# Kernel optimization log

Measured on AMD Instinct MI355X. Metric: run time of the kernel, lower is better.

Reference implementation:

```python
import jax, jax.numpy as jnp
import numpy as np

B, S_BERT, L_WORD, D = 64, 512, 256, 768
REDUC, HID, TAGS, POL = 400, 100, 5, 4


def _make_positions():
    # Each word spans 1-2 consecutive subwords; 256 words * max 2 <= 512 subwords.
    rng = np.random.default_rng(0)
    lens = rng.integers(1, 3, size=(B, L_WORD))          # [B, L] in {1,2}
    starts = np.cumsum(lens, axis=1) - lens              # exclusive prefix sum
    ends = starts + lens - 1                             # inclusive end, <= 511
    return jnp.asarray(np.stack([starts, ends], axis=-1), dtype=jnp.int32)


def setup_inputs() -> dict:
    key = jax.random.key(0)
    ks = jax.random.split(key, 8)
    s = 0.02
    return {
        "bert_vectors": jax.random.normal(ks[0], (B, S_BERT, D), jnp.float32),
        "positions": _make_positions(),
        "W_reduc": jax.random.normal(ks[1], (D, REDUC), jnp.float32) * s,
        "b_reduc": jnp.zeros((REDUC,), jnp.float32),
        "W_ap": jax.random.normal(ks[2], (REDUC, HID), jnp.float32) * s,
        "b_ap": jnp.zeros((HID,), jnp.float32),
        "W_op": jax.random.normal(ks[3], (REDUC, HID), jnp.float32) * s,
        "b_op": jnp.zeros((HID,), jnp.float32),
        "W_ap_tag": jax.random.normal(ks[4], (HID, TAGS), jnp.float32) * s,
        "b_ap_tag": jnp.zeros((TAGS,), jnp.float32),
        "W_op_tag": jax.random.normal(ks[5], (HID, TAGS), jnp.float32) * s,
        "b_op_tag": jnp.zeros((TAGS,), jnp.float32),
        # Biaffine: bias=(True, False) -> in1 gets a ones column: [HID+1, POL*HID]
        "W_bi": jax.random.normal(ks[6], (HID + 1, POL * HID), jnp.float32) * s,
    }


def _segment_mean(vectors, positions):
    # vectors: [B, S, D]; positions: [B, L, 2] inclusive (start, end) spans.
    cs = jnp.cumsum(vectors, axis=1)
    cs = jnp.concatenate([jnp.zeros_like(cs[:, :1]), cs], axis=1)   # [B, S+1, D]
    starts = positions[..., 0]
    ends = positions[..., 1]
    hi = jnp.take_along_axis(cs, (ends + 1)[..., None], axis=1)     # [B, L, D]
    lo = jnp.take_along_axis(cs, starts[..., None], axis=1)
    lens = (ends - starts + 1).astype(vectors.dtype)[..., None]
    return (hi - lo) / lens                                          # [B, L, D]


def reference(bert_vectors, positions, W_reduc, b_reduc, W_ap, b_ap, W_op, b_op,
              W_ap_tag, b_ap_tag, W_op_tag, b_op_tag, W_bi):
    pooled = _segment_mean(bert_vectors, positions)                  # [B, L, D]
    h = jax.nn.relu(pooled @ W_reduc + b_reduc)                      # [B, L, 400]
    ap = jax.nn.relu(h @ W_ap + b_ap)                                # [B, L, 100]
    op = jax.nn.relu(h @ W_op + b_op)                                # [B, L, 100]
    ap_out = ap @ W_ap_tag + b_ap_tag                                # [B, L, T]
    op_out = op @ W_op_tag + b_op_tag                                # [B, L, T]
    # Biaffine with bias=(True, False)
    ones = jnp.ones_like(ap[..., :1])
    a1 = jnp.concatenate([ap, ones], axis=-1)                        # [B, L, 101]
    affine = (a1 @ W_bi).reshape(ap.shape[0], ap.shape[1], POL, HID) # [B, L1, P, H]
    triplet = jnp.einsum('biph,bjh->bjip', affine, op)               # [B, L2, L1, P]
    return ap_out, op_out, triplet
```

## Files before the change

kernel.cpp:

```cpp
#include <hip/hip_runtime.h>
#include <hip/hip_bf16.h>

#define B_    64
#define S_    512
#define L_    256
#define D_    768
#define RED_  400
#define REDP_ 512
#define KEFF_ 416
#define HID_  100
#define HIDP_ 128
#define TAGS_ 5
#define POL_  4
#define NBI_  512
#define NAO_  256
#define BL_   (B_ * L_)

typedef __attribute__((ext_vector_type(8))) short short8;
typedef __attribute__((ext_vector_type(4))) float f32x4;
typedef __attribute__((ext_vector_type(4))) unsigned short u16x4;

#define GLOAD_LDS16(gp, lp) __builtin_amdgcn_global_load_lds( \
    (const __attribute__((address_space(1))) void*)(gp),      \
    (__attribute__((address_space(3))) void*)(lp), 16, 0, 0)

__device__ inline float bf2f(unsigned short u) {
    union { unsigned int i; float f; } c; c.i = ((unsigned)u) << 16; return c.f;
}
__device__ inline unsigned short f2bf(float f) {
    __hip_bfloat16 h = __float2bfloat16(f);
    unsigned short u;
    __builtin_memcpy(&u, &h, 2);
    return u;
}

#define SZ0 393216
#define SZ1 131072
#define SZ2 65536
#define SZ3 512
#define SZ4 256
#define PREP_TOT (SZ0 + SZ1 + SZ2 + SZ3 + SZ4)
#define PREP_BLOCKS ((PREP_TOT + 255) / 256)

__global__ __launch_bounds__(256) void prep_kernel(
    const float* __restrict__ W_reduc, const float* __restrict__ b_reduc,
    const float* __restrict__ W_ap, const float* __restrict__ b_ap,
    const float* __restrict__ W_op, const float* __restrict__ b_op,
    const float* __restrict__ W_bi,
    unsigned short* __restrict__ WtR, unsigned short* __restrict__ WtAO,
    unsigned short* __restrict__ WtBi,
    float* __restrict__ bR, float* __restrict__ bAO, float* __restrict__ bBi)
{
    int idx = blockIdx.x * 256 + threadIdx.x;
    if (idx < SZ0) {
        int n = idx / D_, k = idx - n * D_;
        float v = (n < RED_) ? W_reduc[(size_t)k * RED_ + n] : 0.f;
        WtR[idx] = f2bf(v);
    } else if (idx < SZ0 + SZ1) {
        int i = idx - SZ0;
        int n = i >> 9, k = i & 511;
        float v = 0.f;
        if (k < RED_) {
            if (n < HID_)                      v = W_ap[(size_t)k * HID_ + n];
            else if (n >= 128 && n < 128+HID_) v = W_op[(size_t)k * HID_ + (n-128)];
        }
        WtAO[i] = f2bf(v);
    } else if (idx < SZ0 + SZ1 + SZ2) {
        int i = idx - SZ0 - SZ1;
        int n = i >> 7, k = i & 127;
        int p = n >> 7, h = n & 127;
        float v = (h < HID_ && k < HID_) ? W_bi[(size_t)k * RED_ + p * HID_ + h] : 0.f;
        WtBi[i] = f2bf(v);
        if (k == 0) bBi[n] = (h < HID_) ? W_bi[(size_t)HID_ * RED_ + p * HID_ + h] : 0.f;
    } else if (idx < SZ0 + SZ1 + SZ2 + SZ3) {
        int n = idx - SZ0 - SZ1 - SZ2;
        bR[n] = (n < RED_) ? b_reduc[n] : 0.f;
    } else if (idx < PREP_TOT) {
        int n = idx - SZ0 - SZ1 - SZ2 - SZ3;
        bAO[n] = (n < 128) ? ((n < HID_) ? b_ap[n] : 0.f)
                           : (((n-128) < HID_) ? b_op[n-128] : 0.f);
    }
}

__global__ __launch_bounds__(256) void gemm1_seg_kernel(
    const float* __restrict__ bert, const int* __restrict__ pos,
    const short* __restrict__ Bt, const float* __restrict__ bias,
    unsigned short* __restrict__ Co)
{
    __shared__ __align__(16) short lds[2][10240];

    const int t  = threadIdx.x;
    const int wv = t >> 6;
    const int ln = t & 63;
    const int bm  = blockIdx.x * 64;
    const int bnh = blockIdx.y * 256;
    const int batch = bm >> 8;

    const int srow = t >> 2;
    const int skc  = (t & 3) * 8;

    const int r = bm + srow;
    const int s = pos[r * 2 + 0];
    const int e = pos[r * 2 + 1];
    const size_t rb0 = ((size_t)batch * S_ + s) * D_;
    const size_t rb1 = ((size_t)batch * S_ + e) * D_;

    f32x4 acc[4][4] = {};
    const int NT = D_ >> 5;

    {
        #pragma unroll
        for (int q = 0; q < 4; ++q) {
            const short* g = Bt + (size_t)(bnh + q * 64 + srow) * D_ + skc;
            GLOAD_LDS16(g, &lds[0][2048 + q * 2048 + wv * 512]);
        }
        f32x4 x0 = *(const f32x4*)(bert + rb0 + skc);
        f32x4 x1 = *(const f32x4*)(bert + rb0 + skc + 4);
        f32x4 y0 = *(const f32x4*)(bert + rb1 + skc);
        f32x4 y1 = *(const f32x4*)(bert + rb1 + skc + 4);
        f32x4 s0 = (x0 + y0) * 0.5f;
        f32x4 s1 = (x1 + y1) * 0.5f;
        union { short8 v; unsigned short u[8]; } o;
        #pragma unroll
        for (int j = 0; j < 4; ++j) { o.u[j] = f2bf(s0[j]); o.u[4+j] = f2bf(s1[j]); }
        *(short8*)(&lds[0][srow * 32 + skc]) = o.v;
    }
    __syncthreads();

    int cur = 0;
    const int lr = ln & 15;
    const int lk = (ln >> 4) * 8;

    for (int kt = 0; kt < NT; ++kt) {
        const bool more = (kt + 1 < NT);
        f32x4 x0, x1, y0, y1;
        if (more) {
            int col = (kt + 1) * 32 + skc;
            x0 = *(const f32x4*)(bert + rb0 + col);
            x1 = *(const f32x4*)(bert + rb0 + col + 4);
            y0 = *(const f32x4*)(bert + rb1 + col);
            y1 = *(const f32x4*)(bert + rb1 + col + 4);
            #pragma unroll
            for (int q = 0; q < 4; ++q) {
                const short* g = Bt + (size_t)(bnh + q * 64 + srow) * D_ + (kt + 1) * 32 + skc;
                GLOAD_LDS16(g, &lds[cur ^ 1][2048 + q * 2048 + wv * 512]);
            }
        }

        const short* As = &lds[cur][0];
        const short* Bs = &lds[cur][2048];
        short8 a[4], b[4];
        #pragma unroll
        for (int fi = 0; fi < 4; ++fi)
            a[fi] = *(const short8*)(As + (fi * 16 + lr) * 32 + lk);
        #pragma unroll
        for (int fj = 0; fj < 4; ++fj)
            b[fj] = *(const short8*)(Bs + (wv * 64 + fj * 16 + lr) * 32 + lk);
        #pragma unroll
        for (int fi = 0; fi < 4; ++fi)
            #pragma unroll
            for (int fj = 0; fj < 4; ++fj)
                acc[fi][fj] = __builtin_amdgcn_mfma_f32_16x16x32_bf16(
                    a[fi], b[fj], acc[fi][fj], 0, 0, 0);

        if (more) {
            f32x4 s0 = (x0 + y0) * 0.5f;
            f32x4 s1 = (x1 + y1) * 0.5f;
            union { short8 v; unsigned short u[8]; } o;
            #pragma unroll
            for (int j = 0; j < 4; ++j) { o.u[j] = f2bf(s0[j]); o.u[4+j] = f2bf(s1[j]); }
            *(short8*)(&lds[cur ^ 1][srow * 32 + skc]) = o.v;
        }

        __syncthreads();
        cur ^= 1;
    }

    const int row0 = bm + (ln >> 4) * 4;
    const int col0 = bnh + wv * 64 + lr;
    #pragma unroll
    for (int fi = 0; fi < 4; ++fi)
        #pragma unroll
        for (int rr = 0; rr < 4; ++rr) {
            int row = row0 + fi * 16 + rr;
            #pragma unroll
            for (int fj = 0; fj < 4; ++fj) {
                int col = col0 + fj * 16;
                float v = fmaxf(acc[fi][fj][rr] + bias[col], 0.f);
                Co[(size_t)row * REDP_ + col] = f2bf(v);
            }
        }
}

__global__ __launch_bounds__(256) void gemm23_tag_kernel(
    const short* __restrict__ A, const short* __restrict__ Bt,
    const float* __restrict__ bias,
    unsigned short* __restrict__ apOut, unsigned short* __restrict__ opOut,
    const float* __restrict__ Wap_tag, const float* __restrict__ bap_tag,
    const float* __restrict__ Wop_tag, const float* __restrict__ bop_tag,
    float* __restrict__ out_tag)
{
    __shared__ __align__(16) short lds[2][8192];
    __shared__ float tagf[128 * 101];
    __shared__ float Wtag[HID_ * TAGS_];
    __shared__ float Btag[TAGS_];

    const int t  = threadIdx.x;
    const int wv = t >> 6;
    const int ln = t & 63;
    const int wm = wv >> 1;
    const int wn = wv & 1;
    const int bm = blockIdx.x * 128;
    const int bn = blockIdx.y * 128;
    const int half = blockIdx.y;

    const float* Wt = half ? Wop_tag : Wap_tag;
    const float* bt = half ? bop_tag : bap_tag;
    for (int i = t; i < HID_ * TAGS_; i += 256) Wtag[i] = Wt[i];
    if (t < TAGS_) Btag[t] = bt[t];

    const int srow = t >> 2;
    const int skc  = (t & 3) * 8;
    const int NT = KEFF_ >> 5;

    f32x4 acc[4][4] = {};

    {
        #pragma unroll
        for (int q = 0; q < 2; ++q) {
            const short* g = A + (size_t)(bm + q * 64 + srow) * REDP_ + skc;
            GLOAD_LDS16(g, &lds[0][q * 2048 + wv * 512]);
        }
        #pragma unroll
        for (int q = 0; q < 2; ++q) {
            const short* g = Bt + (size_t)(bn + q * 64 + srow) * REDP_ + skc;
            GLOAD_LDS16(g, &lds[0][4096 + q * 2048 + wv * 512]);
        }
    }
    __syncthreads();

    int cur = 0;
    const int lr = ln & 15;
    const int lk = (ln >> 4) * 8;

    for (int kt = 0; kt < NT; ++kt) {
        if (kt + 1 < NT) {
            int k0 = (kt + 1) << 5;
            #pragma unroll
            for (int q = 0; q < 2; ++q) {
                const short* g = A + (size_t)(bm + q * 64 + srow) * REDP_ + k0 + skc;
                GLOAD_LDS16(g, &lds[cur ^ 1][q * 2048 + wv * 512]);
            }
            #pragma unroll
            for (int q = 0; q < 2; ++q) {
                const short* g = Bt + (size_t)(bn + q * 64 + srow) * REDP_ + k0 + skc;
                GLOAD_LDS16(g, &lds[cur ^ 1][4096 + q * 2048 + wv * 512]);
            }
        }

        const short* As = &lds[cur][0];
        const short* Bs = &lds[cur][4096];
        short8 a[4], b[4];
        #pragma unroll
        for (int fi = 0; fi < 4; ++fi)
            a[fi] = *(const short8*)(As + (wm * 64 + fi * 16 + lr) * 32 + lk);
        #pragma unroll
        for (int fj = 0; fj < 4; ++fj)
            b[fj] = *(const short8*)(Bs + (wn * 64 + fj * 16 + lr) * 32 + lk);
        #pragma unroll
        for (int fi = 0; fi < 4; ++fi)
            #pragma unroll
            for (int fj = 0; fj < 4; ++fj)
                acc[fi][fj] = __builtin_amdgcn_mfma_f32_16x16x32_bf16(
                    a[fi], b[fj], acc[fi][fj], 0, 0, 0);

        __syncthreads();
        cur ^= 1;
    }

    unsigned short* Co = half ? opOut : apOut;
    const int rl0 = wm * 64 + (ln >> 4) * 4;
    const int cl0 = wn * 64 + lr;
    #pragma unroll
    for (int fi = 0; fi < 4; ++fi)
        #pragma unroll
        for (int r = 0; r < 4; ++r) {
            int rl = rl0 + fi * 16 + r;
            #pragma unroll
            for (int fj = 0; fj < 4; ++fj) {
                int cl = cl0 + fj * 16;
                float v = fmaxf(acc[fi][fj][r] + bias[bn + cl], 0.f);
                Co[(size_t)(bm + rl) * 128 + cl] = f2bf(v);
                if (cl < 101) tagf[rl * 101 + cl] = v;
            }
        }
    __syncthreads();

    if (t < 128) {
        float s[TAGS_];
        #pragma unroll
        for (int g = 0; g < TAGS_; ++g) s[g] = Btag[g];
        const float* rowp = &tagf[t * 101];
        for (int k = 0; k < HID_; ++k) {
            float x = rowp[k];
            #pragma unroll
            for (int g = 0; g < TAGS_; ++g) s[g] += x * Wtag[k * TAGS_ + g];
        }
        float* o = out_tag + (size_t)half * (BL_ * TAGS_) + (size_t)(bm + t) * TAGS_;
        #pragma unroll
        for (int g = 0; g < TAGS_; ++g) o[g] = s[g];
    }
}

__global__ __launch_bounds__(256) void bi_triplet_kernel(
    const short* __restrict__ op, const short* __restrict__ ap,
    const short* __restrict__ WtBi, const float* __restrict__ bBi,
    float* __restrict__ out)
{
    __shared__ __align__(16) short As[16384];
    __shared__ __align__(16) short Bs[16384];
    __shared__ __align__(16) short Aap[4096];

    const int t  = threadIdx.x;
    const int wv = t >> 6;
    const int ln = t & 63;
    const int wm = wv >> 1;
    const int wn = wv & 1;
    const int ipt = blockIdx.x;
    const int b   = blockIdx.y;

    const short* opB = op + (size_t)b * 256 * HIDP_;
    const short* apB = ap + ((size_t)b * 256 + ipt * 32) * HIDP_;

    const int rsub = ln >> 2;
    const int j8   = (ln & 3) * 8;

    #pragma unroll
    for (int i = 0; i < 8; ++i) {
        int ks = i >> 1, hf = i & 1;
        int rloc = wv * 32 + hf * 16;
        const short* gA = opB + (size_t)(rloc + rsub) * HIDP_ + ks * 32 + j8;
        GLOAD_LDS16(gA, &As[ks * 4096 + rloc * 32]);
    }
    #pragma unroll
    for (int q = 0; q < 2; ++q) {
        int kf   = q * 2 + (wv >> 1);
        int irow = (wv & 1) * 16 + (ln >> 2);
        const short* gA = apB + (size_t)irow * HIDP_ + kf * 32 + (ln & 3) * 8;
        GLOAD_LDS16(gA, &Aap[q * 2048 + wv * 512]);
    }
    __syncthreads();

    const int lr = ln & 15;
    const int lk = (ln >> 4) * 8;
    const int hbase = wv * 32;

    #pragma unroll
    for (int p = 0; p < 4; ++p) {
        f32x4 acc2[2][2] = {};
        const short* Wp = WtBi + (size_t)(p * 128) * HIDP_;
        #pragma unroll
        for (int kf = 0; kf < 4; ++kf) {
            short8 a2[2], b2[2];
            #pragma unroll
            for (int fm = 0; fm < 2; ++fm)
                a2[fm] = *(const short8*)(Aap + kf * 1024 + (fm * 16 + lr) * 32 + lk);
            #pragma unroll
            for (int fn = 0; fn < 2; ++fn)
                b2[fn] = *(const short8*)(Wp + (size_t)(hbase + fn * 16 + lr) * HIDP_ + kf * 32 + lk);
            #pragma unroll
            for (int fm = 0; fm < 2; ++fm)
                #pragma unroll
                for (int fn = 0; fn < 2; ++fn)
                    acc2[fm][fn] = __builtin_amdgcn_mfma_f32_16x16x32_bf16(
                        a2[fm], b2[fn], acc2[fm][fn], 0, 0, 0);
        }
        #pragma unroll
        for (int fm = 0; fm < 2; ++fm)
            #pragma unroll
            for (int fn = 0; fn < 2; ++fn) {
                int h = hbase + fn * 16 + lr;
                float bias = bBi[p * 128 + h];
                #pragma unroll
                for (int r = 0; r < 4; ++r) {
                    int i = fm * 16 + (ln >> 4) * 4 + r;
                    float v = acc2[fm][fn][r] + bias;
                    Bs[(h >> 5) * 4096 + (i * 4 + p) * 32 + (h & 31)] = (short)f2bf(v);
                }
            }
    }
    __syncthreads();

    float* Ob = out + (size_t)b * 256 * 1024;
    #pragma unroll
    for (int jt = 0; jt < 2; ++jt) {
        f32x4 acc[4][4] = {};
        #pragma unroll
        for (int ks = 0; ks < 4; ++ks) {
            short8 a[4], bf[4];
            #pragma unroll
            for (int fi = 0; fi < 4; ++fi)
                a[fi] = *(const short8*)(As + ks * 4096 + (wm * 64 + fi * 16 + lr) * 32 + lk);
            #pragma unroll
            for (int fj = 0; fj < 4; ++fj)
                bf[fj] = *(const short8*)(Bs + ks * 4096 + (wn * 64 + fj * 16 + lr) * 32 + lk);
            #pragma unroll
            for (int fi = 0; fi < 4; ++fi)
                #pragma unroll
                for (int fj = 0; fj < 4; ++fj)
                    acc[fi][fj] = __builtin_amdgcn_mfma_f32_16x16x32_bf16(
                        a[fi], bf[fj], acc[fi][fj], 0, 0, 0);
        }

        if (jt == 0) {
            __syncthreads();
            #pragma unroll
            for (int i = 0; i < 8; ++i) {
                int ks = i >> 1, hf = i & 1;
                int rloc = wv * 32 + hf * 16;
                const short* gA = opB + (size_t)(128 + rloc + rsub) * HIDP_ + ks * 32 + j8;
                GLOAD_LDS16(gA, &As[ks * 4096 + rloc * 32]);
            }
        }

        const int row0 = jt * 128 + wm * 64 + (ln >> 4) * 4;
        const int col0 = ipt * 128 + wn * 64 + lr;
        #pragma unroll
        for (int fi = 0; fi < 4; ++fi)
            #pragma unroll
            for (int r = 0; r < 4; ++r) {
                int row = row0 + fi * 16 + r;
                #pragma unroll
                for (int fj = 0; fj < 4; ++fj)
                    Ob[(size_t)row * 1024 + col0 + fj * 16] = acc[fi][fj][r];
            }

        if (jt == 0) __syncthreads();
    }
}

extern "C" void kernel_launch(void* const* d_in, const int* in_sizes, int n_in,
                              void* d_out, int out_size, void* d_ws, size_t ws_size,
                              hipStream_t stream)
{
    const float* bert     = (const float*)d_in[0];
    const int*   pos      = (const int*)  d_in[1];
    const float* W_reduc  = (const float*)d_in[2];
    const float* b_reduc  = (const float*)d_in[3];
    const float* W_ap     = (const float*)d_in[4];
    const float* b_ap     = (const float*)d_in[5];
    const float* W_op     = (const float*)d_in[6];
    const float* b_op     = (const float*)d_in[7];
    const float* W_ap_tag = (const float*)d_in[8];
    const float* b_ap_tag = (const float*)d_in[9];
    const float* W_op_tag = (const float*)d_in[10];
    const float* b_op_tag = (const float*)d_in[11];
    const float* W_bi     = (const float*)d_in[12];

    float* out = (float*)d_out;

    char* ws = (char*)d_ws;
    unsigned short* h      = (unsigned short*)ws; ws += (size_t)BL_ * REDP_ * 2;
    unsigned short* ap     = (unsigned short*)ws; ws += (size_t)BL_ * HIDP_ * 2;
    unsigned short* opv    = (unsigned short*)ws; ws += (size_t)BL_ * HIDP_ * 2;
    unsigned short* WtR    = (unsigned short*)ws; ws += (size_t)REDP_ * D_ * 2;
    unsigned short* WtAO   = (unsigned short*)ws; ws += (size_t)NAO_ * REDP_ * 2;
    unsigned short* WtBi   = (unsigned short*)ws; ws += (size_t)NBI_ * HIDP_ * 2;
    float* bR  = (float*)ws;  ws += REDP_ * 4;
    float* bAO = (float*)ws;  ws += NAO_ * 4;
    float* bBi = (float*)ws;  ws += NBI_ * 4;

    prep_kernel<<<PREP_BLOCKS, 256, 0, stream>>>(
        W_reduc, b_reduc, W_ap, b_ap, W_op, b_op, W_bi,
        WtR, WtAO, WtBi, bR, bAO, bBi);

    gemm1_seg_kernel<<<dim3(BL_ / 64, 2), 256, 0, stream>>>(
        bert, pos, (const short*)WtR, bR, h);

    gemm23_tag_kernel<<<dim3(BL_ / 128, 2), 256, 0, stream>>>(
        (const short*)h, (const short*)WtAO, bAO, ap, opv,
        W_ap_tag, b_ap_tag, W_op_tag, b_op_tag, out);

    bi_triplet_kernel<<<dim3(8, B_), 256, 0, stream>>>(
        (const short*)opv, (const short*)ap, (const short*)WtBi, bBi,
        out + 2 * BL_ * TAGS_);
}
```

Before: 77.14 us.

## Retile segment GEMM to 128x128 blocks and vectorize triplet output stores

The first GEMM changes from 64x256 tiles with four waves along N to 128x128 tiles in a 2x2 wave grid. Each thread now gathers two pooled rows and loads half as many weight rows per K step, which shrinks LDS use and changes the grid shape. In the triplet kernel the MFMA operands are swapped so each accumulator holds four consecutive output columns, letting results be written as 16-byte vector stores instead of scalar strided stores. The retile trades occupancy and per-thread gather load against reuse, and the swap relies on the transposed fragment layout matching the output layout.

New measurement: 80.84 us. 4.8% more time.

```diff
diff --git a/kernel.cpp b/kernel.cpp
--- a/kernel.cpp
+++ b/kernel.cpp
@@ -87,43 +87,52 @@
     const short* __restrict__ Bt, const float* __restrict__ bias,
     unsigned short* __restrict__ Co)
 {
-    __shared__ __align__(16) short lds[2][10240];
+    __shared__ __align__(16) short lds[2][8192];
 
     const int t  = threadIdx.x;
     const int wv = t >> 6;
     const int ln = t & 63;
-    const int bm  = blockIdx.x * 64;
-    const int bnh = blockIdx.y * 256;
+    const int wm = wv >> 1;
+    const int wn = wv & 1;
+    const int bm = blockIdx.x * 128;
+    const int bn = blockIdx.y * 128;
     const int batch = bm >> 8;
 
     const int srow = t >> 2;
     const int skc  = (t & 3) * 8;
 
-    const int r = bm + srow;
-    const int s = pos[r * 2 + 0];
-    const int e = pos[r * 2 + 1];
-    const size_t rb0 = ((size_t)batch * S_ + s) * D_;
-    const size_t rb1 = ((size_t)batch * S_ + e) * D_;
+    size_t rb0[2], rb1[2];
+    #pragma unroll
+    for (int q = 0; q < 2; ++q) {
+        int r = bm + q * 64 + srow;
+        int s = pos[r * 2 + 0];
+        int e = pos[r * 2 + 1];
+        rb0[q] = ((size_t)batch * S_ + s) * D_;
+        rb1[q] = ((size_t)batch * S_ + e) * D_;
+    }
 
     f32x4 acc[4][4] = {};
     const int NT = D_ >> 5;
 
     {
         #pragma unroll
-        for (int q = 0; q < 4; ++q) {
-            const short* g = Bt + (size_t)(bnh + q * 64 + srow) * D_ + skc;
-            GLOAD_LDS16(g, &lds[0][2048 + q * 2048 + wv * 512]);
-        }
-        f32x4 x0 = *(const f32x4*)(bert + rb0 + skc);
-        f32x4 x1 = *(const f32x4*)(bert + rb0 + skc + 4);
-        f32x4 y0 = *(const f32x4*)(bert + rb1 + skc);
-        f32x4 y1 = *(const f32x4*)(bert + rb1 + skc + 4);
-        f32x4 s0 = (x0 + y0) * 0.5f;
-        f32x4 s1 = (x1 + y1) * 0.5f;
-        union { short8 v; unsigned short u[8]; } o;
-        #pragma unroll
-        for (int j = 0; j < 4; ++j) { o.u[j] = f2bf(s0[j]); o.u[4+j] = f2bf(s1[j]); }
-        *(short8*)(&lds[0][srow * 32 + skc]) = o.v;
+        for (int q = 0; q < 2; ++q) {
+            const short* g = Bt + (size_t)(bn + q * 64 + srow) * D_ + skc;
+            GLOAD_LDS16(g, &lds[0][4096 + q * 2048 + wv * 512]);
+        }
+        #pragma unroll
+        for (int q = 0; q < 2; ++q) {
+            f32x4 x0 = *(const f32x4*)(bert + rb0[q] + skc);
+            f32x4 x1 = *(const f32x4*)(bert + rb0[q] + skc + 4);
+            f32x4 y0 = *(const f32x4*)(bert + rb1[q] + skc);
+            f32x4 y1 = *(const f32x4*)(bert + rb1[q] + skc + 4);
+            f32x4 s0 = (x0 + y0) * 0.5f;
+            f32x4 s1 = (x1 + y1) * 0.5f;
+            union { short8 v; unsigned short u[8]; } o;
+            #pragma unroll
+            for (int j = 0; j < 4; ++j) { o.u[j] = f2bf(s0[j]); o.u[4+j] = f2bf(s1[j]); }
+            *(short8*)(&lds[0][(q * 64 + srow) * 32 + skc]) = o.v;
+        }
     }
     __syncthreads();
 
@@ -133,29 +142,32 @@
 
     for (int kt = 0; kt < NT; ++kt) {
         const bool more = (kt + 1 < NT);
-        f32x4 x0, x1, y0, y1;
+        f32x4 x0[2], x1[2], y0[2], y1[2];
         if (more) {
             int col = (kt + 1) * 32 + skc;
-            x0 = *(const f32x4*)(bert + rb0 + col);
-            x1 = *(const f32x4*)(bert + rb0 + col + 4);
-            y0 = *(const f32x4*)(bert + rb1 + col);
-            y1 = *(const f32x4*)(bert + rb1 + col + 4);
-            #pragma unroll
-            for (int q = 0; q < 4; ++q) {
-                const short* g = Bt + (size_t)(bnh + q * 64 + srow) * D_ + (kt + 1) * 32 + skc;
-                GLOAD_LDS16(g, &lds[cur ^ 1][2048 + q * 2048 + wv * 512]);
+            #pragma unroll
+            for (int q = 0; q < 2; ++q) {
+                x0[q] = *(const f32x4*)(bert + rb0[q] + col);
+                x1[q] = *(const f32x4*)(bert + rb0[q] + col + 4);
+                y0[q] = *(const f32x4*)(bert + rb1[q] + col);
+                y1[q] = *(const f32x4*)(bert + rb1[q] + col + 4);
+            }
+            #pragma unroll
+            for (int q = 0; q < 2; ++q) {
+                const short* g = Bt + (size_t)(bn + q * 64 + srow) * D_ + (kt + 1) * 32 + skc;
+                GLOAD_LDS16(g, &lds[cur ^ 1][4096 + q * 2048 + wv * 512]);
             }
         }
 
         const short* As = &lds[cur][0];
-        const short* Bs = &lds[cur][2048];
+        const short* Bs = &lds[cur][4096];
         short8 a[4], b[4];
         #pragma unroll
         for (int fi = 0; fi < 4; ++fi)
-            a[fi] = *(const short8*)(As + (fi * 16 + lr) * 32 + lk);
+            a[fi] = *(const short8*)(As + (wm * 64 + fi * 16 + lr) * 32 + lk);
         #pragma unroll
         for (int fj = 0; fj < 4; ++fj)
-            b[fj] = *(const short8*)(Bs + (wv * 64 + fj * 16 + lr) * 32 + lk);
+            b[fj] = *(const short8*)(Bs + (wn * 64 + fj * 16 + lr) * 32 + lk);
         #pragma unroll
         for (int fi = 0; fi < 4; ++fi)
             #pragma unroll
@@ -164,20 +176,23 @@
                     a[fi], b[fj], acc[fi][fj], 0, 0, 0);
 
         if (more) {
-            f32x4 s0 = (x0 + y0) * 0.5f;
-            f32x4 s1 = (x1 + y1) * 0.5f;
-            union { short8 v; unsigned short u[8]; } o;
-            #pragma unroll
-            for (int j = 0; j < 4; ++j) { o.u[j] = f2bf(s0[j]); o.u[4+j] = f2bf(s1[j]); }
-            *(short8*)(&lds[cur ^ 1][srow * 32 + skc]) = o.v;
+            #pragma unroll
+            for (int q = 0; q < 2; ++q) {
+                f32x4 s0 = (x0[q] + y0[q]) * 0.5f;
+                f32x4 s1 = (x1[q] + y1[q]) * 0.5f;
+                union { short8 v; unsigned short u[8]; } o;
+                #pragma unroll
+                for (int j = 0; j < 4; ++j) { o.u[j] = f2bf(s0[j]); o.u[4+j] = f2bf(s1[j]); }
+                *(short8*)(&lds[cur ^ 1][(q * 64 + srow) * 32 + skc]) = o.v;
+            }
         }
 
         __syncthreads();
         cur ^= 1;
     }
 
-    const int row0 = bm + (ln >> 4) * 4;
-    const int col0 = bnh + wv * 64 + lr;
+    const int row0 = bm + wm * 64 + (ln >> 4) * 4;
+    const int col0 = bn + wn * 64 + lr;
     #pragma unroll
     for (int fi = 0; fi < 4; ++fi)
         #pragma unroll
@@ -397,19 +412,19 @@
         f32x4 acc[4][4] = {};
         #pragma unroll
         for (int ks = 0; ks < 4; ++ks) {
-            short8 a[4], bf[4];
-            #pragma unroll
-            for (int fi = 0; fi < 4; ++fi)
-                a[fi] = *(const short8*)(As + ks * 4096 + (wm * 64 + fi * 16 + lr) * 32 + lk);
-            #pragma unroll
-            for (int fj = 0; fj < 4; ++fj)
-                bf[fj] = *(const short8*)(Bs + ks * 4096 + (wn * 64 + fj * 16 + lr) * 32 + lk);
-            #pragma unroll
-            for (int fi = 0; fi < 4; ++fi)
+            short8 af[4], of[4];
+            #pragma unroll
+            for (int fa = 0; fa < 4; ++fa)
+                af[fa] = *(const short8*)(Bs + ks * 4096 + (wn * 64 + fa * 16 + lr) * 32 + lk);
+            #pragma unroll
+            for (int fo = 0; fo < 4; ++fo)
+                of[fo] = *(const short8*)(As + ks * 4096 + (wm * 64 + fo * 16 + lr) * 32 + lk);
+            #pragma unroll
+            for (int fa = 0; fa < 4; ++fa)
                 #pragma unroll
-                for (int fj = 0; fj < 4; ++fj)
-                    acc[fi][fj] = __builtin_amdgcn_mfma_f32_16x16x32_bf16(
-                        a[fi], bf[fj], acc[fi][fj], 0, 0, 0);
+                for (int fo = 0; fo < 4; ++fo)
+                    acc[fa][fo] = __builtin_amdgcn_mfma_f32_16x16x32_bf16(
+                        af[fa], of[fo], acc[fa][fo], 0, 0, 0);
         }
 
         if (jt == 0) {
@@ -423,17 +438,17 @@
             }
         }
 
-        const int row0 = jt * 128 + wm * 64 + (ln >> 4) * 4;
-        const int col0 = ipt * 128 + wn * 64 + lr;
-        #pragma unroll
-        for (int fi = 0; fi < 4; ++fi)
-            #pragma unroll
-            for (int r = 0; r < 4; ++r) {
-                int row = row0 + fi * 16 + r;
-                #pragma unroll
-                for (int fj = 0; fj < 4; ++fj)
-                    Ob[(size_t)row * 1024 + col0 + fj * 16] = acc[fi][fj][r];
-            }
+        const int jb  = jt * 128 + wm * 64 + lr;
+        const int ipb = ipt * 128 + wn * 64 + (ln >> 4) * 4;
+        #pragma unroll
+        for (int fa = 0; fa < 4; ++fa) {
+            int ip0 = ipb + fa * 16;
+            #pragma unroll
+            for (int fo = 0; fo < 4; ++fo) {
+                int j = jb + fo * 16;
+                *(f32x4*)(Ob + (size_t)j * 1024 + ip0) = acc[fa][fo];
+            }
+        }
 
         if (jt == 0) __syncthreads();
     }
@@ -474,7 +489,7 @@
         W_reduc, b_reduc, W_ap, b_ap, W_op, b_op, W_bi,
         WtR, WtAO, WtBi, bR, bAO, bBi);
 
-    gemm1_seg_kernel<<<dim3(BL_ / 64, 2), 256, 0, stream>>>(
+    gemm1_seg_kernel<<<dim3(BL_ / 128, REDP_ / 128), 256, 0, stream>>>(
         bert, pos, (const short*)WtR, bR, h);
 
     gemm23_tag_kernel<<<dim3(BL_ / 128, 2), 256, 0, stream>>>(
```

## Shrink gemm1 N-tile to 128 with 2x2 waves; vectorize triplet output stores

Applied to the files above, without the earlier changes.

The segment-mean GEMM now uses a 64x128 tile with a 2x2 wave layout instead of 64x256, which doubles the grid along N and roughly halves LDS and accumulator registers per block. That should raise occupancy, at the cost of recomputing the bert segment loads once per N-block. The triplet kernel swaps the MFMA operand roles so each lane's accumulator holds four consecutive output columns, so the fp32 output can be written with 16-byte vector stores instead of scalar strided stores.

After: 87.42 us. 13.3% more time.

```diff
diff --git a/kernel.cpp b/kernel.cpp
--- a/kernel.cpp
+++ b/kernel.cpp
@@ -87,13 +87,15 @@
     const short* __restrict__ Bt, const float* __restrict__ bias,
     unsigned short* __restrict__ Co)
 {
-    __shared__ __align__(16) short lds[2][10240];
+    __shared__ __align__(16) short lds[2][6144];
 
     const int t  = threadIdx.x;
     const int wv = t >> 6;
     const int ln = t & 63;
-    const int bm  = blockIdx.x * 64;
-    const int bnh = blockIdx.y * 256;
+    const int wm = wv >> 1;
+    const int wn = wv & 1;
+    const int bm = blockIdx.x * 64;
+    const int bn = blockIdx.y * 128;
     const int batch = bm >> 8;
 
     const int srow = t >> 2;
@@ -105,13 +107,13 @@
     const size_t rb0 = ((size_t)batch * S_ + s) * D_;
     const size_t rb1 = ((size_t)batch * S_ + e) * D_;
 
-    f32x4 acc[4][4] = {};
+    f32x4 acc[2][4] = {};
     const int NT = D_ >> 5;
 
     {
         #pragma unroll
-        for (int q = 0; q < 4; ++q) {
-            const short* g = Bt + (size_t)(bnh + q * 64 + srow) * D_ + skc;
+        for (int q = 0; q < 2; ++q) {
+            const short* g = Bt + (size_t)(bn + q * 64 + srow) * D_ + skc;
             GLOAD_LDS16(g, &lds[0][2048 + q * 2048 + wv * 512]);
         }
         f32x4 x0 = *(const f32x4*)(bert + rb0 + skc);
@@ -141,23 +143,23 @@
             y0 = *(const f32x4*)(bert + rb1 + col);
             y1 = *(const f32x4*)(bert + rb1 + col + 4);
             #pragma unroll
-            for (int q = 0; q < 4; ++q) {
-                const short* g = Bt + (size_t)(bnh + q * 64 + srow) * D_ + (kt + 1) * 32 + skc;
+            for (int q = 0; q < 2; ++q) {
+                const short* g = Bt + (size_t)(bn + q * 64 + srow) * D_ + (kt + 1) * 32 + skc;
                 GLOAD_LDS16(g, &lds[cur ^ 1][2048 + q * 2048 + wv * 512]);
             }
         }
 
         const short* As = &lds[cur][0];
         const short* Bs = &lds[cur][2048];
-        short8 a[4], b[4];
-        #pragma unroll
-        for (int fi = 0; fi < 4; ++fi)
-            a[fi] = *(const short8*)(As + (fi * 16 + lr) * 32 + lk);
+        short8 a[2], b[4];
+        #pragma unroll
+        for (int fi = 0; fi < 2; ++fi)
+            a[fi] = *(const short8*)(As + (wm * 32 + fi * 16 + lr) * 32 + lk);
         #pragma unroll
         for (int fj = 0; fj < 4; ++fj)
-            b[fj] = *(const short8*)(Bs + (wv * 64 + fj * 16 + lr) * 32 + lk);
-        #pragma unroll
-        for (int fi = 0; fi < 4; ++fi)
+            b[fj] = *(const short8*)(Bs + (wn * 64 + fj * 16 + lr) * 32 + lk);
+        #pragma unroll
+        for (int fi = 0; fi < 2; ++fi)
             #pragma unroll
             for (int fj = 0; fj < 4; ++fj)
                 acc[fi][fj] = __builtin_amdgcn_mfma_f32_16x16x32_bf16(
@@ -176,10 +178,10 @@
         cur ^= 1;
     }
 
-    const int row0 = bm + (ln >> 4) * 4;
-    const int col0 = bnh + wv * 64 + lr;
-    #pragma unroll
-    for (int fi = 0; fi < 4; ++fi)
+    const int row0 = bm + wm * 32 + (ln >> 4) * 4;
+    const int col0 = bn + wn * 64 + lr;
+    #pragma unroll
+    for (int fi = 0; fi < 2; ++fi)
         #pragma unroll
         for (int rr = 0; rr < 4; ++rr) {
             int row = row0 + fi * 16 + rr;
@@ -397,19 +399,19 @@
         f32x4 acc[4][4] = {};
         #pragma unroll
         for (int ks = 0; ks < 4; ++ks) {
-            short8 a[4], bf[4];
-            #pragma unroll
-            for (int fi = 0; fi < 4; ++fi)
-                a[fi] = *(const short8*)(As + ks * 4096 + (wm * 64 + fi * 16 + lr) * 32 + lk);
-            #pragma unroll
-            for (int fj = 0; fj < 4; ++fj)
-                bf[fj] = *(const short8*)(Bs + ks * 4096 + (wn * 64 + fj * 16 + lr) * 32 + lk);
-            #pragma unroll
-            for (int fi = 0; fi < 4; ++fi)
+            short8 af[4], of[4];
+            #pragma unroll
+            for (int fa = 0; fa < 4; ++fa)
+                af[fa] = *(const short8*)(Bs + ks * 4096 + (wn * 64 + fa * 16 + lr) * 32 + lk);
+            #pragma unroll
+            for (int fo = 0; fo < 4; ++fo)
+                of[fo] = *(const short8*)(As + ks * 4096 + (wm * 64 + fo * 16 + lr) * 32 + lk);
+            #pragma unroll
+            for (int fa = 0; fa < 4; ++fa)
                 #pragma unroll
-                for (int fj = 0; fj < 4; ++fj)
-                    acc[fi][fj] = __builtin_amdgcn_mfma_f32_16x16x32_bf16(
-                        a[fi], bf[fj], acc[fi][fj], 0, 0, 0);
+                for (int fo = 0; fo < 4; ++fo)
+                    acc[fa][fo] = __builtin_amdgcn_mfma_f32_16x16x32_bf16(
+                        af[fa], of[fo], acc[fa][fo], 0, 0, 0);
         }
 
         if (jt == 0) {
@@ -423,17 +425,17 @@
             }
         }
 
-        const int row0 = jt * 128 + wm * 64 + (ln >> 4) * 4;
-        const int col0 = ipt * 128 + wn * 64 + lr;
-        #pragma unroll
-        for (int fi = 0; fi < 4; ++fi)
-            #pragma unroll
-            for (int r = 0; r < 4; ++r) {
-                int row = row0 + fi * 16 + r;
-                #pragma unroll
-                for (int fj = 0; fj < 4; ++fj)
-                    Ob[(size_t)row * 1024 + col0 + fj * 16] = acc[fi][fj][r];
-            }
+        const int jb  = jt * 128 + wm * 64 + lr;
+        const int ipb = ipt * 128 + wn * 64 + (ln >> 4) * 4;
+        #pragma unroll
+        for (int fa = 0; fa < 4; ++fa) {
+            int ip0 = ipb + fa * 16;
+            #pragma unroll
+            for (int fo = 0; fo < 4; ++fo) {
+                int j = jb + fo * 16;
+                *(f32x4*)(Ob + (size_t)j * 1024 + ip0) = acc[fa][fo];
+            }
+        }
 
         if (jt == 0) __syncthreads();
     }
@@ -474,7 +476,7 @@
         W_reduc, b_reduc, W_ap, b_ap, W_op, b_op, W_bi,
         WtR, WtAO, WtBi, bR, bAO, bBi);
 
-    gemm1_seg_kernel<<<dim3(BL_ / 64, 2), 256, 0, stream>>>(
+    gemm1_seg_kernel<<<dim3(BL_ / 64, REDP_ / 128), 256, 0, stream>>>(
         bert, pos, (const short*)WtR, bR, h);
 
     gemm23_tag_kernel<<<dim3(BL_ / 128, 2), 256, 0, stream>>>(
```
